# Performance work log

Measured on AMD Instinct MI355X. Metric: run time of the kernel, lower is better.

## Reference

```python
import jax, jax.numpy as jnp
import numpy as np

B, S, D, H = 4, 2048, 512, 8
E = D // H  # d_head = 64

def setup_inputs() -> dict:
    key = jax.random.key(0)
    ks = jax.random.split(key, 10)
    s_in = (1.0 / np.sqrt(D))
    x  = jax.random.normal(ks[0], (B, S, D), dtype=jnp.float32)
    Wq = jax.random.normal(ks[1], (H, D, E), dtype=jnp.float32) * s_in
    bq = jax.random.normal(ks[2], (H, E), dtype=jnp.float32) * 0.01
    Wk = jax.random.normal(ks[3], (H, D, E), dtype=jnp.float32) * s_in
    bk = jax.random.normal(ks[4], (H, E), dtype=jnp.float32) * 0.01
    Wv = jax.random.normal(ks[5], (H, D, E), dtype=jnp.float32) * s_in
    bv = jax.random.normal(ks[6], (H, E), dtype=jnp.float32) * 0.01
    Wo = jax.random.normal(ks[7], (D, D), dtype=jnp.float32) * s_in
    bo = jax.random.normal(ks[8], (D,), dtype=jnp.float32) * 0.01
    return {"x": x, "Wq": Wq, "bq": bq, "Wk": Wk, "bk": bk,
            "Wv": Wv, "bv": bv, "Wo": Wo, "bo": bo}

def reference(x, Wq, bq, Wk, bk, Wv, bv, Wo, bo):
    B_, S_, D_ = x.shape
    # per-head projections (batched over head axis h)
    q = jnp.einsum('bsd,hde->bhse', x, Wq) + bq[None, :, None, :]
    k = jnp.einsum('bsd,hde->bhse', x, Wk) + bk[None, :, None, :]
    v = jnp.einsum('bsd,hde->bhse', x, Wv) + bv[None, :, None, :]
    # NOTE: original scales by d_model**-0.5 (full D), not d_head**-0.5
    scale = jnp.asarray(D_, x.dtype) ** -0.5
    scores = jnp.einsum('bhse,bhte->bhst', q, k) * scale  # [B,H,S,S]
    causal = jnp.tril(jnp.ones((S_, S_), dtype=bool))
    scores = jnp.where(causal[None, None], scores, -jnp.inf)
    attn = jax.nn.softmax(scores, axis=-1)
    out = jnp.einsum('bhst,bhte->bhse', attn, v)  # [B,H,S,E]
    # concat heads along feature dim (head-major), matching torch.cat
    out = out.transpose(0, 2, 1, 3).reshape(B_, S_, D_)
    return out @ Wo + bo  # final projection; dropout never applied in source
```

## Files before the change

kernel.cpp:

```cpp
#include <hip/hip_runtime.h>

typedef unsigned short u16;
typedef __bf16 bf16x8 __attribute__((ext_vector_type(8)));
typedef short s16x4 __attribute__((ext_vector_type(4)));
typedef short s16x8 __attribute__((ext_vector_type(8)));
typedef float f32x4 __attribute__((ext_vector_type(4)));

#define BB 4
#define SS 2048
#define DD 512
#define HH 8
#define EE 64
#define MM 8192
#define BHSE (BB*HH*SS*EE)

#define GLOBAL_AS __attribute__((address_space(1)))
#define LDS_AS    __attribute__((address_space(3)))

__device__ __forceinline__ float b2f(u16 u) {
    return __uint_as_float(((unsigned int)u) << 16);
}
__device__ __forceinline__ u16 f2b(float f) {
    unsigned int v = __float_as_uint(f);
    v += 0x7fffu + ((v >> 16) & 1u);
    return (u16)(v >> 16);
}
__device__ __forceinline__ float loadE(const void* p, size_t idx, int isbf16) {
    return isbf16 ? b2f(((const u16*)p)[idx]) : ((const float*)p)[idx];
}
__device__ __forceinline__ f32x4 mfma16x16x16_bf16(s16x4 a, s16x4 b, f32x4 c) {
    return __builtin_amdgcn_mfma_f32_16x16x16bf16_1k(a, b, c, 0, 0, 0);
}
__device__ __forceinline__ void load_lds16(const u16* g, u16* l) {
    __builtin_amdgcn_global_load_lds((GLOBAL_AS void*)g, (LDS_AS void*)l, 16, 0, 0);
}

__device__ __forceinline__ int detect_bf16(const u16* x) {
    int sane = 0;
    for (int i = 0; i < 128; ++i) {
        float a = fabsf(b2f(x[2 * i]));
        if (a == 0.f || (a > 1e-4f && a < 100.f)) ++sane;
    }
    return sane >= 96;
}

__global__ __launch_bounds__(256) void convert_x(
    const void* __restrict__ X, u16* __restrict__ Xb, int* __restrict__ flag)
{
    const int isbf16 = detect_bf16((const u16*)X);
    if (blockIdx.x == 0 && threadIdx.x == 0) *flag = isbf16;
    const size_t i0 = ((size_t)blockIdx.x * 256 + threadIdx.x) * 16;
    if (isbf16) {
        const uint4* src = (const uint4*)(((const u16*)X) + i0);
        uint4* dst = (uint4*)(Xb + i0);
        dst[0] = src[0];
        dst[1] = src[1];
    } else {
        const float* xf = ((const float*)X) + i0;
        float4 f0 = *(const float4*)xf;
        float4 f1 = *(const float4*)(xf + 4);
        float4 f2 = *(const float4*)(xf + 8);
        float4 f3 = *(const float4*)(xf + 12);
        u16 tmp[16] = { f2b(f0.x), f2b(f0.y), f2b(f0.z), f2b(f0.w),
                        f2b(f1.x), f2b(f1.y), f2b(f1.z), f2b(f1.w),
                        f2b(f2.x), f2b(f2.y), f2b(f2.z), f2b(f2.w),
                        f2b(f3.x), f2b(f3.y), f2b(f3.z), f2b(f3.w) };
        *(uint4*)(Xb + i0) = *(const uint4*)tmp;
        *(uint4*)(Xb + i0 + 8) = *(const uint4*)(tmp + 8);
    }
}

__global__ __launch_bounds__(256) void transpose_weights(
    const void* __restrict__ Wq, const void* __restrict__ Wk,
    const void* __restrict__ Wv, const void* __restrict__ Wo,
    u16* __restrict__ WT, u16* __restrict__ WoT, const int* __restrict__ flag)
{
    const int isbf16 = *flag;
    const int j = blockIdx.x;
    const int job = j >> 6;
    const int t = j & 63;
    const void* src; u16* dst; int src_ld, dst_ld;
    if (job < 3) {
        const void* W = (job == 0) ? Wq : ((job == 1) ? Wk : Wv);
        int h = t >> 3, kt = t & 7;
        size_t off = (size_t)h * DD * EE + (size_t)kt * 64 * EE;
        src = isbf16 ? (const void*)(((const u16*)W) + off)
                     : (const void*)(((const float*)W) + off);
        src_ld = EE;
        dst = WT + (size_t)job * 512 * 512 + (size_t)(h * 64) * 512 + kt * 64;
        dst_ld = 512;
    } else {
        int a = t >> 3, b = t & 7;
        size_t off = (size_t)(a * 64) * 512 + b * 64;
        src = isbf16 ? (const void*)(((const u16*)Wo) + off)
                     : (const void*)(((const float*)Wo) + off);
        src_ld = 512;
        dst = WoT + (size_t)(b * 64) * 512 + a * 64;
        dst_ld = 512;
    }
    __shared__ __align__(16) u16 Ts[64 * 72];
    const int tid = threadIdx.x;
#pragma unroll
    for (int it = 0; it < 2; ++it) {
        int idx = it * 256 + tid;
        int r = idx >> 3, c = (idx & 7) << 3;
#pragma unroll
        for (int k = 0; k < 8; ++k) {
            float v = loadE(src, (size_t)r * src_ld + c + k, isbf16);
            Ts[(c + k) * 72 + r] = f2b(v);
        }
    }
    __syncthreads();
#pragma unroll
    for (int it = 0; it < 2; ++it) {
        int idx = it * 256 + tid;
        int r = idx >> 3, c = (idx & 7) << 3;
        *(bf16x8*)(dst + (size_t)r * dst_ld + c) = *(const bf16x8*)&Ts[r * 72 + c];
    }
}

template<int MT, int NT>
__device__ __forceinline__ void mfma_step(const u16* As, const u16* Bs,
    int mh, int nh, int lq, int quad, f32x4 acc[MT][NT])
{
    const int sw = lq & 7;
#pragma unroll
    for (int kw = 0; kw < 2; ++kw) {
        const int G = kw * 4 + quad;
        const int col = ((G ^ sw) << 3);
        bf16x8 a[MT], b[NT];
#pragma unroll
        for (int mt = 0; mt < MT; ++mt)
            a[mt] = *(const bf16x8*)&As[(mh + mt * 16 + lq) * 64 + col];
#pragma unroll
        for (int nt = 0; nt < NT; ++nt)
            b[nt] = *(const bf16x8*)&Bs[(nh + nt * 16 + lq) * 64 + col];
#pragma unroll
        for (int mt = 0; mt < MT; ++mt)
#pragma unroll
            for (int nt = 0; nt < NT; ++nt)
                acc[mt][nt] = __builtin_amdgcn_mfma_f32_16x16x32_bf16(a[mt], b[nt], acc[mt][nt], 0, 0, 0);
    }
}

__global__ __launch_bounds__(256) void gemm_qkv(
    const u16* __restrict__ Xb, const u16* __restrict__ WT,
    const void* __restrict__ bq, const void* __restrict__ bk,
    const void* __restrict__ bv, u16* __restrict__ qkv,
    const int* __restrict__ flag)
{
    const float SCALE = 0.04419417382415922f;
    const int isbf16 = *flag;
    const int l = blockIdx.x;
    const int m0 = ((l & 7) * 8 + ((l >> 3) & 7)) * 128;
    const int n0 = (l >> 6) * 128;
    const int tid = threadIdx.x;
    const int wave = tid >> 6, lane = tid & 63;
    const int lq = lane & 15, quad = lane >> 4;
    const int mh = (wave & 1) * 64, nh = (wave >> 1) * 64;
    __shared__ __align__(16) u16 As[128 * 64];
    __shared__ __align__(16) u16 Bs[128 * 64];
    f32x4 acc[4][4] = {};

    const int swz = (lane & 7) ^ ((lane >> 3) & 7);
    const size_t lane_off = (size_t)(lane >> 3) * 512 + 8 * swz;

    for (int k0 = 0; k0 < 512; k0 += 64) {
        __syncthreads();
#pragma unroll
        for (int jj = 0; jj < 4; ++jj) {
            const int c = wave * 4 + jj;
            load_lds16(Xb + (size_t)(m0 + 8 * c) * 512 + k0 + lane_off, &As[c * 512]);
            load_lds16(WT + (size_t)(n0 + 8 * c) * 512 + k0 + lane_off, &Bs[c * 512]);
        }
        __syncthreads();
        mfma_step<4, 4>(As, Bs, mh, nh, lq, quad, acc);
    }

    const int proj = n0 >> 9;
    const void* bias = (proj == 0) ? bq : ((proj == 1) ? bk : bv);
#pragma unroll
    for (int mt = 0; mt < 4; ++mt) {
#pragma unroll
        for (int nt = 0; nt < 4; ++nt) {
#pragma unroll
            for (int r = 0; r < 4; ++r) {
                int m = m0 + mh + mt * 16 + quad * 4 + r;
                int n = n0 + nh + nt * 16 + lq;
                int nn = n & 511;
                float v = acc[mt][nt][r] + loadE(bias, nn, isbf16);
                if (proj == 0) v *= SCALE;
                int b_ = m >> 11, s = m & 2047, h = nn >> 6, e = nn & 63;
                qkv[(size_t)proj * BHSE + (((size_t)(b_ * HH + h) * SS + s) * EE + e)] = f2b(v);
            }
        }
    }
}

struct Stage { uint4 k0, k1, va, vb; };

__device__ __forceinline__ void stage_load(Stage& st, const u16* Kh, const u16* Vh,
                                           int t0, int tid) {
    int r = tid >> 3, c = (tid & 7) * 8;
    st.k0 = *(const uint4*)(Kh + (size_t)(t0 + r) * 64 + c);
    st.k1 = *(const uint4*)(Kh + (size_t)(t0 + r + 32) * 64 + c);
    int t2 = 2 * (tid & 31), e8 = (tid >> 5) * 8;
    st.va = *(const uint4*)(Vh + (size_t)(t0 + t2) * 64 + e8);
    st.vb = *(const uint4*)(Vh + (size_t)(t0 + t2 + 1) * 64 + e8);
}
__device__ __forceinline__ void stage_write(const Stage& st, u16* Ksb, u16* VTsb, int tid) {
    int r = tid >> 3, c = (tid & 7) * 8;
    *(uint4*)(Ksb + r * 72 + c) = st.k0;
    *(uint4*)(Ksb + (r + 32) * 72 + c) = st.k1;
    int t2 = 2 * (tid & 31), e8 = (tid >> 5) * 8;
    int g2 = ((t2 >> 2) & 3) * 16 + ((t2 >> 4) << 2) + (t2 & 3);
    const unsigned* pa = (const unsigned*)&st.va;
    const unsigned* pb = (const unsigned*)&st.vb;
#pragma unroll
    for (int k = 0; k < 4; ++k) {
        unsigned lo = __builtin_amdgcn_perm(pb[k], pa[k], 0x05040100u);
        unsigned hi = __builtin_amdgcn_perm(pb[k], pa[k], 0x07060302u);
        *(unsigned*)(VTsb + (e8 + 2 * k) * 72 + g2) = lo;
        *(unsigned*)(VTsb + (e8 + 2 * k + 1) * 72 + g2) = hi;
    }
}

__device__ __forceinline__ void attn_tile(const u16* Ksb, const u16* VTsb,
    bf16x8 qf0, bf16x8 qf1, int lq, int quad, int wave, bool diag,
    f32x4 Ot[4], float& lacc)
{
#pragma unroll
    for (int half = 0; half < 2; ++half) {
        s16x4 vf[4][2];
#pragma unroll
        for (int et = 0; et < 4; ++et) {
            const u16* Vp = VTsb + (et * 16 + lq) * 72 + quad * 16 + half * 8;
            s16x8 v = *(const s16x8*)Vp;
            vf[et][0] = __builtin_shufflevector(v, v, 0, 1, 2, 3);
            vf[et][1] = __builtin_shufflevector(v, v, 4, 5, 6, 7);
        }
#pragma unroll
        for (int tj = 0; tj < 2; ++tj) {
            const int tt = half * 2 + tj;
            const u16* Krow = Ksb + (tt * 16 + lq) * 72;
            bf16x8 k0 = *(const bf16x8*)(Krow + quad * 8);
            bf16x8 k1 = *(const bf16x8*)(Krow + 32 + quad * 8);
            f32x4 sc = {};
            sc = __builtin_amdgcn_mfma_f32_16x16x32_bf16(k0, qf0, sc, 0, 0, 0);
            sc = __builtin_amdgcn_mfma_f32_16x16x32_bf16(k1, qf1, sc, 0, 0, 0);
            unsigned pu[4];
#pragma unroll
            for (int r = 0; r < 4; ++r) {
                float p = __expf(sc[r]);
                if (diag) {
                    int tl = tt * 16 + quad * 4 + r;
                    int ql = 16 * wave + lq;
                    p = (tl <= ql) ? p : 0.f;
                }
                lacc += __uint_as_float(__float_as_uint(p) & 0xffff0000u);
                pu[r] = __float_as_uint(p);
            }
            union { unsigned u[2]; s16x4 s; } pf;
            pf.u[0] = __builtin_amdgcn_perm(pu[1], pu[0], 0x07060302u);
            pf.u[1] = __builtin_amdgcn_perm(pu[3], pu[2], 0x07060302u);
#pragma unroll
            for (int et = 0; et < 4; ++et)
                Ot[et] = mfma16x16x16_bf16(vf[et][tj], pf.s, Ot[et]);
        }
    }
}

__global__ __launch_bounds__(256) void attn_kernel(
    const u16* __restrict__ Qg, const u16* __restrict__ Kg,
    const u16* __restrict__ Vg, u16* __restrict__ Og)
{
    const int bh = blockIdx.x;
    const int qb = ((int)gridDim.y - 1 - (int)blockIdx.y) * 64;
    const int nt = qb >> 6;
    const int tid = threadIdx.x;
    const int wave = tid >> 6, lane = tid & 63;
    const int lq = lane & 15, quad = lane >> 4;
    const int b = bh >> 3, h = bh & 7;

    const size_t base = (size_t)bh * SS * EE;
    const u16* Kh = Kg + base;
    const u16* Vh = Vg + base;

    __shared__ __align__(16) u16 Ks[2][64 * 72];
    __shared__ __align__(16) u16 VTs[2][64 * 72];

    const int qrow = qb + 16 * wave + lq;
    const u16* Qp = Qg + base + (size_t)qrow * EE;
    bf16x8 qf0 = *(const bf16x8*)(Qp + quad * 8);
    bf16x8 qf1 = *(const bf16x8*)(Qp + 32 + quad * 8);

    f32x4 Ot[4] = {};
    float lacc = 0.f;

    Stage st;
    stage_load(st, Kh, Vh, 0, tid);
    stage_write(st, Ks[0], VTs[0], tid);
    for (int i = 0; i <= nt; ++i) {
        __syncthreads();
        const int cur = i & 1;
        const bool more = (i < nt);
        if (more) stage_load(st, Kh, Vh, (i + 1) * 64, tid);
        attn_tile(Ks[cur], VTs[cur], qf0, qf1, lq, quad, wave, i == nt, Ot, lacc);
        if (more) stage_write(st, Ks[cur ^ 1], VTs[cur ^ 1], tid);
    }

    lacc += __shfl_xor(lacc, 16);
    lacc += __shfl_xor(lacc, 32);
    const float inv = 1.f / lacc;

    u16* Op = Og + (((size_t)(b * SS + qrow)) * HH + h) * EE;
#pragma unroll
    for (int et = 0; et < 4; ++et) {
        u16 tmp[4];
#pragma unroll
        for (int r = 0; r < 4; ++r) tmp[r] = f2b(Ot[et][r] * inv);
        *(uint2*)(Op + et * 16 + quad * 4) = *(const uint2*)tmp;
    }
}

__global__ __launch_bounds__(256) void gemm_out(
    const u16* __restrict__ A, const u16* __restrict__ WoT,
    const void* __restrict__ bo, void* __restrict__ out,
    const int* __restrict__ flag)
{
    const int isbf16 = *flag;
    const int l = blockIdx.x;
    const int m0 = ((l & 7) * 8 + ((l >> 3) & 7)) * 128;
    const int n0 = (l >> 6) * 64;
    const int tid = threadIdx.x;
    const int wave = tid >> 6, lane = tid & 63;
    const int lq = lane & 15, quad = lane >> 4;
    const int mh = (wave & 1) * 64, nh = (wave >> 1) * 32;
    __shared__ __align__(16) u16 As[128 * 64];
    __shared__ __align__(16) u16 Bs[64 * 64];
    f32x4 acc[4][2] = {};

    const int swz = (lane & 7) ^ ((lane >> 3) & 7);
    const size_t lane_off = (size_t)(lane >> 3) * 512 + 8 * swz;

    for (int k0 = 0; k0 < 512; k0 += 64) {
        __syncthreads();
#pragma unroll
        for (int jj = 0; jj < 4; ++jj) {
            const int c = wave * 4 + jj;
            load_lds16(A + (size_t)(m0 + 8 * c) * 512 + k0 + lane_off, &As[c * 512]);
        }
#pragma unroll
        for (int jj = 0; jj < 2; ++jj) {
            const int c = wave * 2 + jj;
            load_lds16(WoT + (size_t)(n0 + 8 * c) * 512 + k0 + lane_off, &Bs[c * 512]);
        }
        __syncthreads();
        mfma_step<4, 2>(As, Bs, mh, nh, lq, quad, acc);
    }
#pragma unroll
    for (int mt = 0; mt < 4; ++mt) {
#pragma unroll
        for (int nt = 0; nt < 2; ++nt) {
#pragma unroll
            for (int r = 0; r < 4; ++r) {
                int m = m0 + mh + mt * 16 + quad * 4 + r;
                int n = n0 + nh + nt * 16 + lq;
                float v = acc[mt][nt][r] + loadE(bo, n, isbf16);
                if (isbf16) ((u16*)out)[(size_t)m * 512 + n] = f2b(v);
                else        ((float*)out)[(size_t)m * 512 + n] = v;
            }
        }
    }
}

extern "C" void kernel_launch(void* const* d_in, const int* in_sizes, int n_in,
                              void* d_out, int out_size, void* d_ws, size_t ws_size,
                              hipStream_t stream) {
    const void* x  = d_in[0];
    const void* Wq = d_in[1];
    const void* bq = d_in[2];
    const void* Wk = d_in[3];
    const void* bk = d_in[4];
    const void* Wv = d_in[5];
    const void* bv = d_in[6];
    const void* Wo = d_in[7];
    const void* bo = d_in[8];

    u16* WT   = (u16*)d_ws;
    u16* WoT  = WT + 3 * 512 * 512;
    u16* qkv  = WoT + 512 * 512;
    u16* attn = qkv + 3 * (size_t)BHSE;
    int* flag = (int*)(attn + (size_t)BHSE);
    u16* Xb   = (u16*)(flag + 8);

    convert_x<<<MM * DD / (256 * 16), 256, 0, stream>>>(x, Xb, flag);
    transpose_weights<<<256, 256, 0, stream>>>(Wq, Wk, Wv, Wo, WT, WoT, flag);
    gemm_qkv<<<(MM / 128) * (1536 / 128), 256, 0, stream>>>(Xb, WT, bq, bk, bv, qkv, flag);
    attn_kernel<<<dim3(BB * HH, SS / 64), 256, 0, stream>>>(qkv, qkv + BHSE, qkv + 2 * (size_t)BHSE, attn);
    gemm_out<<<(MM / 128) * (512 / 64), 256, 0, stream>>>(attn, WoT, bo, d_out, flag);
}
```

Measured before the change: 201.9 us.

## Merge prep kernels, vectorize weight transpose, compute softmax denominator via MFMA

Fuses convert_x and transpose_weights into one prep kernel, which removes a launch and the dependency on the flag written by a previous kernel. bf16 detection now uses a wave ballot instead of a 128-iteration serial loop per thread. Weight loads in the transpose are vectorized. In attention, the row-sum of probabilities is accumulated by an extra MFMA against a ones vector, replacing the per-element scalar adds and the final shuffles. This adds one MFMA per tile, which could compete with the matrix pipeline.

```diff
diff --git a/kernel.cpp b/kernel.cpp
--- a/kernel.cpp
+++ b/kernel.cpp
@@ -35,51 +35,53 @@
     __builtin_amdgcn_global_load_lds((GLOBAL_AS void*)g, (LDS_AS void*)l, 16, 0, 0);
 }
 
-__device__ __forceinline__ int detect_bf16(const u16* x) {
-    int sane = 0;
-    for (int i = 0; i < 128; ++i) {
-        float a = fabsf(b2f(x[2 * i]));
-        if (a == 0.f || (a > 1e-4f && a < 100.f)) ++sane;
-    }
-    return sane >= 96;
-}
-
-__global__ __launch_bounds__(256) void convert_x(
-    const void* __restrict__ X, u16* __restrict__ Xb, int* __restrict__ flag)
-{
-    const int isbf16 = detect_bf16((const u16*)X);
-    if (blockIdx.x == 0 && threadIdx.x == 0) *flag = isbf16;
-    const size_t i0 = ((size_t)blockIdx.x * 256 + threadIdx.x) * 16;
-    if (isbf16) {
-        const uint4* src = (const uint4*)(((const u16*)X) + i0);
-        uint4* dst = (uint4*)(Xb + i0);
-        dst[0] = src[0];
-        dst[1] = src[1];
-    } else {
-        const float* xf = ((const float*)X) + i0;
-        float4 f0 = *(const float4*)xf;
-        float4 f1 = *(const float4*)(xf + 4);
-        float4 f2 = *(const float4*)(xf + 8);
-        float4 f3 = *(const float4*)(xf + 12);
-        u16 tmp[16] = { f2b(f0.x), f2b(f0.y), f2b(f0.z), f2b(f0.w),
-                        f2b(f1.x), f2b(f1.y), f2b(f1.z), f2b(f1.w),
-                        f2b(f2.x), f2b(f2.y), f2b(f2.z), f2b(f2.w),
-                        f2b(f3.x), f2b(f3.y), f2b(f3.z), f2b(f3.w) };
-        *(uint4*)(Xb + i0) = *(const uint4*)tmp;
-        *(uint4*)(Xb + i0 + 8) = *(const uint4*)(tmp + 8);
-    }
-}
-
-__global__ __launch_bounds__(256) void transpose_weights(
+__device__ __forceinline__ int detect_bf16_wave(const u16* x) {
+    const int lane = threadIdx.x & 63;
+    float a0 = fabsf(b2f(x[2 * lane]));
+    float a1 = fabsf(b2f(x[2 * (lane + 64)]));
+    int c0 = (a0 == 0.f) || (a0 > 1e-4f && a0 < 100.f);
+    int c1 = (a1 == 0.f) || (a1 > 1e-4f && a1 < 100.f);
+    int cnt = __popcll(__ballot(c0)) + __popcll(__ballot(c1));
+    return cnt >= 96;
+}
+
+__global__ __launch_bounds__(256) void prep(
+    const void* __restrict__ X,
     const void* __restrict__ Wq, const void* __restrict__ Wk,
     const void* __restrict__ Wv, const void* __restrict__ Wo,
-    u16* __restrict__ WT, u16* __restrict__ WoT, const int* __restrict__ flag)
-{
-    const int isbf16 = *flag;
-    const int j = blockIdx.x;
+    u16* __restrict__ Xb, u16* __restrict__ WT, u16* __restrict__ WoT,
+    int* __restrict__ flag)
+{
+    const int isbf16 = detect_bf16_wave((const u16*)X);
+    const int bid = blockIdx.x;
+    const int tid = threadIdx.x;
+    if (bid < 1024) {
+        if (bid == 0 && tid == 0) *flag = isbf16;
+        const size_t i0 = ((size_t)bid * 256 + tid) * 16;
+        if (isbf16) {
+            const uint4* src = (const uint4*)(((const u16*)X) + i0);
+            uint4* dst = (uint4*)(Xb + i0);
+            dst[0] = src[0];
+            dst[1] = src[1];
+        } else {
+            const float* xf = ((const float*)X) + i0;
+            float4 f0 = *(const float4*)xf;
+            float4 f1 = *(const float4*)(xf + 4);
+            float4 f2 = *(const float4*)(xf + 8);
+            float4 f3 = *(const float4*)(xf + 12);
+            u16 tmp[16] = { f2b(f0.x), f2b(f0.y), f2b(f0.z), f2b(f0.w),
+                            f2b(f1.x), f2b(f1.y), f2b(f1.z), f2b(f1.w),
+                            f2b(f2.x), f2b(f2.y), f2b(f2.z), f2b(f2.w),
+                            f2b(f3.x), f2b(f3.y), f2b(f3.z), f2b(f3.w) };
+            *(uint4*)(Xb + i0) = *(const uint4*)tmp;
+            *(uint4*)(Xb + i0 + 8) = *(const uint4*)(tmp + 8);
+        }
+        return;
+    }
+    const int j = bid - 1024;
     const int job = j >> 6;
     const int t = j & 63;
-    const void* src; u16* dst; int src_ld, dst_ld;
+    const void* src; u16* dst; int src_ld;
     if (job < 3) {
         const void* W = (job == 0) ? Wq : ((job == 1) ? Wk : Wv);
         int h = t >> 3, kt = t & 7;
@@ -88,7 +90,6 @@
                      : (const void*)(((const float*)W) + off);
         src_ld = EE;
         dst = WT + (size_t)job * 512 * 512 + (size_t)(h * 64) * 512 + kt * 64;
-        dst_ld = 512;
     } else {
         int a = t >> 3, b = t & 7;
         size_t off = (size_t)(a * 64) * 512 + b * 64;
@@ -96,26 +97,31 @@
                      : (const void*)(((const float*)Wo) + off);
         src_ld = 512;
         dst = WoT + (size_t)(b * 64) * 512 + a * 64;
-        dst_ld = 512;
     }
     __shared__ __align__(16) u16 Ts[64 * 72];
-    const int tid = threadIdx.x;
 #pragma unroll
     for (int it = 0; it < 2; ++it) {
         int idx = it * 256 + tid;
         int r = idx >> 3, c = (idx & 7) << 3;
-#pragma unroll
-        for (int k = 0; k < 8; ++k) {
-            float v = loadE(src, (size_t)r * src_ld + c + k, isbf16);
-            Ts[(c + k) * 72 + r] = f2b(v);
-        }
+        u16 tmp[8];
+        if (isbf16) {
+            *(bf16x8*)tmp = *(const bf16x8*)(((const u16*)src) + (size_t)r * src_ld + c);
+        } else {
+            const float* sp = ((const float*)src) + (size_t)r * src_ld + c;
+            float4 f0 = *(const float4*)sp;
+            float4 f1 = *(const float4*)(sp + 4);
+            tmp[0] = f2b(f0.x); tmp[1] = f2b(f0.y); tmp[2] = f2b(f0.z); tmp[3] = f2b(f0.w);
+            tmp[4] = f2b(f1.x); tmp[5] = f2b(f1.y); tmp[6] = f2b(f1.z); tmp[7] = f2b(f1.w);
+        }
+#pragma unroll
+        for (int k = 0; k < 8; ++k) Ts[(c + k) * 72 + r] = tmp[k];
     }
     __syncthreads();
 #pragma unroll
     for (int it = 0; it < 2; ++it) {
         int idx = it * 256 + tid;
         int r = idx >> 3, c = (idx & 7) << 3;
-        *(bf16x8*)(dst + (size_t)r * dst_ld + c) = *(const bf16x8*)&Ts[r * 72 + c];
+        *(bf16x8*)(dst + (size_t)r * 512 + c) = *(const bf16x8*)&Ts[r * 72 + c];
     }
 }
 
@@ -227,8 +233,9 @@
 
 __device__ __forceinline__ void attn_tile(const u16* Ksb, const u16* VTsb,
     bf16x8 qf0, bf16x8 qf1, int lq, int quad, int wave, bool diag,
-    f32x4 Ot[4], float& lacc)
-{
+    f32x4 Ot[4], f32x4& lfrag)
+{
+    const s16x4 ones = { (short)0x3F80, (short)0x3F80, (short)0x3F80, (short)0x3F80 };
 #pragma unroll
     for (int half = 0; half < 2; ++half) {
         s16x4 vf[4][2];
@@ -257,12 +264,12 @@
                     int ql = 16 * wave + lq;
                     p = (tl <= ql) ? p : 0.f;
                 }
-                lacc += __uint_as_float(__float_as_uint(p) & 0xffff0000u);
                 pu[r] = __float_as_uint(p);
             }
             union { unsigned u[2]; s16x4 s; } pf;
             pf.u[0] = __builtin_amdgcn_perm(pu[1], pu[0], 0x07060302u);
             pf.u[1] = __builtin_amdgcn_perm(pu[3], pu[2], 0x07060302u);
+            lfrag = mfma16x16x16_bf16(ones, pf.s, lfrag);
 #pragma unroll
             for (int et = 0; et < 4; ++et)
                 Ot[et] = mfma16x16x16_bf16(vf[et][tj], pf.s, Ot[et]);
@@ -295,7 +302,7 @@
     bf16x8 qf1 = *(const bf16x8*)(Qp + 32 + quad * 8);
 
     f32x4 Ot[4] = {};
-    float lacc = 0.f;
+    f32x4 lfrag = {};
 
     Stage st;
     stage_load(st, Kh, Vh, 0, tid);
@@ -305,13 +312,11 @@
         const int cur = i & 1;
         const bool more = (i < nt);
         if (more) stage_load(st, Kh, Vh, (i + 1) * 64, tid);
-        attn_tile(Ks[cur], VTs[cur], qf0, qf1, lq, quad, wave, i == nt, Ot, lacc);
+        attn_tile(Ks[cur], VTs[cur], qf0, qf1, lq, quad, wave, i == nt, Ot, lfrag);
         if (more) stage_write(st, Ks[cur ^ 1], VTs[cur ^ 1], tid);
     }
 
-    lacc += __shfl_xor(lacc, 16);
-    lacc += __shfl_xor(lacc, 32);
-    const float inv = 1.f / lacc;
+    const float inv = 1.f / lfrag[0];
 
     u16* Op = Og + (((size_t)(b * SS + qrow)) * HH + h) * EE;
 #pragma unroll
@@ -394,8 +399,7 @@
     int* flag = (int*)(attn + (size_t)BHSE);
     u16* Xb   = (u16*)(flag + 8);
 
-    convert_x<<<MM * DD / (256 * 16), 256, 0, stream>>>(x, Xb, flag);
-    transpose_weights<<<256, 256, 0, stream>>>(Wq, Wk, Wv, Wo, WT, WoT, flag);
+    prep<<<1024 + 256, 256, 0, stream>>>(x, Wq, Wk, Wv, Wo, Xb, WT, WoT, flag);
     gemm_qkv<<<(MM / 128) * (1536 / 128), 256, 0, stream>>>(Xb, WT, bq, bk, bv, qkv, flag);
     attn_kernel<<<dim3(BB * HH, SS / 64), 256, 0, stream>>>(qkv, qkv + BHSE, qkv + 2 * (size_t)BHSE, attn);
     gemm_out<<<(MM / 128) * (512 / 64), 256, 0, stream>>>(attn, WoT, bo, d_out, flag);
```

After: 188.7 us. 6.5% less time.
